# Performance work log

Hardware: AMD Instinct MI355X
Metric: run time of the kernel (lower is better)

The kernel has to match this reference:

```python
import jax, jax.numpy as jnp
import numpy as np

# Config (matches init_kwargs)
B, C, H, W = 32, 128, 12, 1200   # z: (B, in_dim, H, W)
DIN = C * H                       # 1536
FIX = 768                         # get_multiple(DIN // 2, 6)
OV = 4                            # overlap
G = 6                             # num_vqs
D = OV * FIX // G                 # 512 per-group embedding size (all equal)
K = 1024                          # codebook_size
COMMIT = 0.25


def setup_inputs() -> dict:
    key = jax.random.key(0)
    k1, k2, k3, k4 = jax.random.split(key, 4)
    z = jax.random.normal(k1, (B, C, H, W), dtype=jnp.float32)
    w_down = jax.random.normal(k2, (FIX, DIN), dtype=jnp.float32) * 0.02
    w_up = jax.random.normal(k3, (DIN, FIX), dtype=jnp.float32) * 0.02
    embedding = jax.random.normal(k4, (G, D, K), dtype=jnp.float32)  # per-group (embedding_size, num_embedding)
    return {"z": z, "w_down": w_down, "w_up": w_up, "embedding": embedding}


def _quantize_group(zg, emb):
    # zg: (B, T, D), emb: (D, K)
    zf = zg.reshape(-1, D)
    # squared euclidean distance: |z|^2 - 2 z@E + |E|^2 -> (N, K)
    dist = (zf * zf).sum(1, keepdims=True) - 2.0 * (zf @ emb) + (emb * emb).sum(0, keepdims=True)
    idx = jnp.argmin(dist, axis=1)            # (N,)
    q = jnp.take(emb.T, idx, axis=0).reshape(zg.shape)
    # straight-through estimator (training mode)
    zq = zg + jax.lax.stop_gradient(q - zg)
    loss = COMMIT * jnp.mean((jax.lax.stop_gradient(zq) - zg) ** 2)
    return zq, loss


def reference(z, w_down, w_up, embedding):
    # pre_process: (B,C,H,W) -> permute(0,2,3,1) -> permute(0,2,3,1) -> (B, W, C*H)
    x = jnp.transpose(z, (0, 3, 1, 2)).reshape(B, W, DIN)  # (B, W, C, H) flattened
    x = x @ w_down.T                                       # proj_down -> (B, W, FIX)
    T = W // OV
    x = x.reshape(B, T, OV * FIX)                          # (B, T, 3072)
    # split into G contiguous groups of size D along last axis -> (G, B, T, D)
    xg = jnp.transpose(x.reshape(B, T, G, D), (2, 0, 1, 3))
    zq_g, losses = jax.vmap(_quantize_group)(xg, embedding)
    vq_loss = losses.sum() / G
    # concat groups back -> (B, T, G*D)
    zq = jnp.transpose(zq_g, (1, 2, 0, 3)).reshape(B, T, G * D)
    # post_process: un-overlap, proj_up, back to (B, C, H, W)
    zq = zq.reshape(B, W, FIX)
    zq = zq @ w_up.T                                       # (B, W, DIN)
    zq = zq.reshape(B, W, C, H)
    zq = jnp.transpose(zq, (0, 3, 1, 2))                   # (B, H, W, C)
    zq = jnp.transpose(zq, (0, 3, 1, 2))                   # dim==4 -> (B, C, H, W)
    return zq, vq_loss
```

## Files before the change

### kernel.cpp

```cpp
#include <hip/hip_runtime.h>

#define BB 32
#define CC 128
#define HH 12
#define WW 1200
#define DIN 1536
#define FIXD 768
#define OVL 4
#define GG 6
#define DD 512
#define KK 1024
#define TT 300
#define NV 9600
#define MROWS 38400

#define Y_OFF     0
#define ET_OFF    29491200
#define NORM_OFF  32636928
#define BEST_OFF  32643072
#define LOSS_OFF  32758272

__global__ __launch_bounds__(256) void k_gemm_down(const float* __restrict__ z,
                                                   const float* __restrict__ w_down,
                                                   float* __restrict__ Y) {
    __shared__ float As[16][68];
    __shared__ float Bs[16][132];
    const int bm = blockIdx.x, bn = blockIdx.y;
    const int tid = threadIdx.x;
    const int n0 = bm * 64, f0 = bn * 128;
    const int arow = tid & 63;
    const int akk0 = tid >> 6;
    const int nA = n0 + arow;
    const int bA = nA / WW, wA = nA - bA * WW;
    const size_t zbase = (size_t)bA * (CC * HH * WW) + wA;
    const int rbase = (tid >> 4) << 2;
    const int cbase = (tid & 15) << 3;
    float acc[4][8] = {};
    for (int kt = 0; kt < DIN; kt += 16) {
        #pragma unroll
        for (int i = 0; i < 4; i++) {
            int kk = akk0 + i * 4;
            As[kk][arow] = z[zbase + (size_t)(kt + kk) * WW];
        }
        #pragma unroll
        for (int i = 0; i < 2; i++) {
            int fl = tid + i * 256;
            int col = fl >> 2, q = fl & 3;
            const float4 v = *(const float4*)&w_down[(size_t)(f0 + col) * DIN + kt + q * 4];
            Bs[q * 4 + 0][col] = v.x;
            Bs[q * 4 + 1][col] = v.y;
            Bs[q * 4 + 2][col] = v.z;
            Bs[q * 4 + 3][col] = v.w;
        }
        __syncthreads();
        #pragma unroll
        for (int k = 0; k < 16; k++) {
            const float4 a  = *(const float4*)&As[k][rbase];
            const float4 ba = *(const float4*)&Bs[k][cbase];
            const float4 bb = *(const float4*)&Bs[k][cbase + 4];
            const float av[4] = {a.x, a.y, a.z, a.w};
            const float bv[8] = {ba.x, ba.y, ba.z, ba.w, bb.x, bb.y, bb.z, bb.w};
            #pragma unroll
            for (int i = 0; i < 4; i++)
                #pragma unroll
                for (int j = 0; j < 8; j++)
                    acc[i][j] = fmaf(av[i], bv[j], acc[i][j]);
        }
        __syncthreads();
    }
    #pragma unroll
    for (int i = 0; i < 4; i++) {
        float4 o0, o1;
        o0.x = acc[i][0]; o0.y = acc[i][1]; o0.z = acc[i][2]; o0.w = acc[i][3];
        o1.x = acc[i][4]; o1.y = acc[i][5]; o1.z = acc[i][6]; o1.w = acc[i][7];
        float* yr = &Y[(size_t)(n0 + rbase + i) * FIXD + f0 + cbase];
        *(float4*)yr = o0;
        *(float4*)(yr + 4) = o1;
    }
}

__global__ __launch_bounds__(256) void k_transpose(const float* __restrict__ emb,
                                                   float* __restrict__ ET) {
    int i = blockIdx.x * 256 + threadIdx.x;
    if (i >= GG * KK * DD) return;
    int d = i & 511;
    int rem = i >> 9;
    int k = rem & 1023;
    int g = rem >> 10;
    ET[i] = emb[((g * DD + d) << 10) + k];
}

__global__ __launch_bounds__(64) void k_norms(const float* __restrict__ ET,
                                              float* __restrict__ norms) {
    const int code = blockIdx.x;
    const int lane = threadIdx.x;
    const float* row = ET + code * DD;
    double s = 0.0;
    #pragma unroll
    for (int r = 0; r < 8; r++) {
        float v = row[lane + r * 64];
        s += (double)v * (double)v;
    }
    #pragma unroll
    for (int off = 32; off; off >>= 1) s += __shfl_down(s, off);
    if (lane == 0) norms[code] = (float)s;
}

__global__ __launch_bounds__(256) void k_dist2(const float* __restrict__ Y,
                                               const float* __restrict__ ET,
                                               const float* __restrict__ norms,
                                               unsigned long long* __restrict__ best) {
    __shared__ float Zs[16][68];
    __shared__ float Es[16][132];
    __shared__ unsigned long long red[64][17];
    const int vt = blockIdx.x;
    const int ct = blockIdx.y;
    const int g  = blockIdx.z;
    const int tid = threadIdx.x;
    const int rgrp = tid >> 4, cgrp = tid & 15;
    const int rbase = rgrp * 4, cbase = cgrp * 8;
    const int v0 = vt * 64, c0 = ct * 128;
    const float* ETg = ET + (size_t)g * KK * DD;

    const int zrow = tid >> 2, zq = tid & 3;
    const int vz = v0 + zrow;
    const int bz = vz / TT, tz = vz - bz * TT;

    float acc[4][8] = {};

    for (int kt = 0; kt < DD; kt += 16) {
        const int p0 = g * DD + kt;
        const int s = p0 / FIXD, f0 = p0 - s * FIXD;
        {
            const float4 v = *(const float4*)&Y[(bz * WW + tz * OVL + s) * FIXD + f0 + zq * 4];
            Zs[zq * 4 + 0][zrow] = v.x;
            Zs[zq * 4 + 1][zrow] = v.y;
            Zs[zq * 4 + 2][zrow] = v.z;
            Zs[zq * 4 + 3][zrow] = v.w;
        }
        #pragma unroll
        for (int i = 0; i < 2; i++) {
            int flat = tid + i * 256;
            int code = flat >> 2, q = flat & 3;
            const float4 v = *(const float4*)&ETg[(c0 + code) * DD + kt + q * 4];
            Es[q * 4 + 0][code] = v.x;
            Es[q * 4 + 1][code] = v.y;
            Es[q * 4 + 2][code] = v.z;
            Es[q * 4 + 3][code] = v.w;
        }
        __syncthreads();
        #pragma unroll
        for (int k = 0; k < 16; k++) {
            const float4 z4 = *(const float4*)&Zs[k][rbase];
            const float4 ea = *(const float4*)&Es[k][cbase];
            const float4 eb = *(const float4*)&Es[k][cbase + 4];
            const float zv[4] = {z4.x, z4.y, z4.z, z4.w};
            const float ev[8] = {ea.x, ea.y, ea.z, ea.w, eb.x, eb.y, eb.z, eb.w};
            #pragma unroll
            for (int i = 0; i < 4; i++)
                #pragma unroll
                for (int j = 0; j < 8; j++)
                    acc[i][j] = fmaf(zv[i], ev[j], acc[i][j]);
        }
        __syncthreads();
    }

    unsigned long long kbest[4];
    #pragma unroll
    for (int i = 0; i < 4; i++) kbest[i] = ~0ull;
    #pragma unroll
    for (int j = 0; j < 8; j++) {
        const int c = c0 + cbase + j;
        const float nrm = norms[(g << 10) + c];
        #pragma unroll
        for (int i = 0; i < 4; i++) {
            float score = nrm - 2.0f * acc[i][j];
            unsigned u = __float_as_uint(score);
            u = (u & 0x80000000u) ? ~u : (u | 0x80000000u);
            unsigned long long key = ((unsigned long long)u << 32) | (unsigned)c;
            if (key < kbest[i]) kbest[i] = key;
        }
    }
    #pragma unroll
    for (int i = 0; i < 4; i++) red[rbase + i][cgrp] = kbest[i];
    __syncthreads();
    if (tid < 64) {
        unsigned long long b = red[tid][0];
        #pragma unroll
        for (int j = 1; j < 16; j++) {
            unsigned long long v = red[tid][j];
            if (v < b) b = v;
        }
        atomicMin(&best[g * NV + v0 + tid], b);
    }
}

__global__ __launch_bounds__(256) void k_loss(const float* __restrict__ Y,
                                              const float* __restrict__ ET,
                                              const unsigned long long* __restrict__ best,
                                              float* __restrict__ lossAcc) {
    const int total = GG * NV * DD;
    const int stride = gridDim.x * 256;
    float s = 0.0f;
    for (int e = blockIdx.x * 256 + threadIdx.x; e < total; e += stride) {
        int g = e / (NV * DD);
        int r = e - g * (NV * DD);
        int v = r >> 9, d = r & 511;
        int ii = (int)(unsigned)best[g * NV + v];
        float q = ET[((size_t)(g * KK + ii)) * DD + d];
        int b = v / TT, t = v - b * TT;
        int p = g * DD + d;
        int sg = p / FIXD, f = p - sg * FIXD;
        float zv = Y[(b * WW + t * OVL + sg) * FIXD + f];
        float df = q - zv;
        s = fmaf(df, df, s);
    }
    __shared__ float red[256];
    red[threadIdx.x] = s;
    __syncthreads();
    for (int off = 128; off; off >>= 1) {
        if (threadIdx.x < off) red[threadIdx.x] += red[threadIdx.x + off];
        __syncthreads();
    }
    if (threadIdx.x == 0) atomicAdd(lossAcc, red[0]);
}

__constant__ int SEG_G[8]  = {0, 1, 1, 2, 3, 4, 4, 5};
__constant__ int SEG_D0[8] = {0, 0, 256, 0, 0, 0, 256, 0};
__constant__ int SEG_L[8]  = {512, 256, 256, 512, 512, 256, 256, 512};
__constant__ int SEG_F0[8] = {0, 512, 0, 256, 0, 512, 0, 256};

__global__ __launch_bounds__(256) void k_table(const float* __restrict__ ET,
                                               const float* __restrict__ w_up,
                                               float* __restrict__ Tab) {
    __shared__ float As[16][68];
    __shared__ float Bs[16][132];
    const int bm = blockIdx.x;
    const int bn = blockIdx.y;
    const int seg = blockIdx.z;
    const int g = SEG_G[seg], d0 = SEG_D0[seg], len = SEG_L[seg], fb = SEG_F0[seg];
    const int tid = threadIdx.x;
    const int k0 = bm * 64, dout0 = bn * 128;
    const int arow = tid >> 2, aq = tid & 3;
    const int rbase = (tid >> 4) << 2;
    const int cbase = (tid & 15) << 3;
    const float* ETg = ET + (size_t)(g << 10) * DD;
    float acc[4][8] = {};
    for (int kt = 0; kt < len; kt += 16) {
        {
            const float4 v = *(const float4*)&ETg[(size_t)(k0 + arow) * DD + d0 + kt + aq * 4];
            As[aq * 4 + 0][arow] = v.x;
            As[aq * 4 + 1][arow] = v.y;
            As[aq * 4 + 2][arow] = v.z;
            As[aq * 4 + 3][arow] = v.w;
        }
        #pragma unroll
        for (int i = 0; i < 2; i++) {
            int fl = tid + i * 256;
            int col = fl >> 2, q = fl & 3;
            const float4 v = *(const float4*)&w_up[(size_t)(dout0 + col) * FIXD + fb + kt + q * 4];
            Bs[q * 4 + 0][col] = v.x;
            Bs[q * 4 + 1][col] = v.y;
            Bs[q * 4 + 2][col] = v.z;
            Bs[q * 4 + 3][col] = v.w;
        }
        __syncthreads();
        #pragma unroll
        for (int k = 0; k < 16; k++) {
            const float4 a  = *(const float4*)&As[k][rbase];
            const float4 ba = *(const float4*)&Bs[k][cbase];
            const float4 bb = *(const float4*)&Bs[k][cbase + 4];
            const float av[4] = {a.x, a.y, a.z, a.w};
            const float bv[8] = {ba.x, ba.y, ba.z, ba.w, bb.x, bb.y, bb.z, bb.w};
            #pragma unroll
            for (int i = 0; i < 4; i++)
                #pragma unroll
                for (int j = 0; j < 8; j++)
                    acc[i][j] = fmaf(av[i], bv[j], acc[i][j]);
        }
        __syncthreads();
    }
    #pragma unroll
    for (int i = 0; i < 4; i++) {
        float4 o0, o1;
        o0.x = acc[i][0]; o0.y = acc[i][1]; o0.z = acc[i][2]; o0.w = acc[i][3];
        o1.x = acc[i][4]; o1.y = acc[i][5]; o1.z = acc[i][6]; o1.w = acc[i][7];
        float* tr = &Tab[(size_t)((seg << 10) + k0 + rbase + i) * DIN + dout0 + cbase];
        *(float4*)tr = o0;
        *(float4*)(tr + 4) = o1;
    }
}

__global__ __launch_bounds__(256) void k_scatter(const float* __restrict__ Tab,
                                                 const unsigned long long* __restrict__ best,
                                                 float* __restrict__ out) {
    __shared__ float Ls[64][65];
    const int dt = blockIdx.x;
    const int wt = blockIdx.y;
    const int b  = blockIdx.z;
    const int dout0 = dt * 64, w0 = wt * 64;
    const int wlim = (WW - w0 < 64) ? (WW - w0) : 64;
    const int tid = threadIdx.x;
    const int wi = tid >> 2, q = tid & 3;

    int se = 0;
    size_t rowE = 0, rowO = 0;
    if (wi < wlim) {
        const int w = w0 + wi;
        const int s = w & 3;
        const int t = w >> 2;
        const int gEt[4] = {0, 1, 3, 4};
        const int gOt[4] = {1, 2, 4, 5};
        int ce = (int)(unsigned)best[gEt[s] * NV + b * TT + t];
        int co = (int)(unsigned)best[gOt[s] * NV + b * TT + t];
        se = s;
        rowE = (size_t)(((2 * s) << 10) + ce) * DIN;
        rowO = (size_t)(((2 * s + 1) << 10) + co) * DIN;
    }
    if (wi < wlim) {
        #pragma unroll
        for (int rep = 0; rep < 4; rep++) {
            const int doff = rep * 16 + q * 4;
            const float4 a = *(const float4*)&Tab[rowE + dout0 + doff];
            const float4 c = *(const float4*)&Tab[rowO + dout0 + doff];
            Ls[wi][doff + 0] = a.x + c.x;
            Ls[wi][doff + 1] = a.y + c.y;
            Ls[wi][doff + 2] = a.z + c.z;
            Ls[wi][doff + 3] = a.w + c.w;
        }
    }
    __syncthreads();
    const size_t obase = (size_t)b * (CC * HH * WW) + (size_t)dout0 * WW + w0;
    #pragma unroll
    for (int i = 0; i < 16; i++) {
        int flat = tid + i * 256;
        int dr = flat >> 6, wj = flat & 63;
        if (wj < wlim) out[obase + (size_t)dr * WW + wj] = Ls[wj][dr];
    }
}

__global__ void k_finish(const float* __restrict__ lossAcc, float* __restrict__ out) {
    if (threadIdx.x == 0)
        out[58982400] = lossAcc[0] * (0.25f / 29491200.0f);
}

extern "C" void kernel_launch(void* const* d_in, const int* in_sizes, int n_in,
                              void* d_out, int out_size, void* d_ws, size_t ws_size,
                              hipStream_t stream) {
    const float* z      = (const float*)d_in[0];
    const float* w_down = (const float*)d_in[1];
    const float* w_up   = (const float*)d_in[2];
    const float* emb    = (const float*)d_in[3];
    float* out = (float*)d_out;

    float* ws    = (float*)d_ws;
    float* Y     = ws + Y_OFF;
    float* Tab   = ws + Y_OFF;
    float* ET    = ws + ET_OFF;
    float* norms = ws + NORM_OFF;
    unsigned long long* best = (unsigned long long*)(ws + BEST_OFF);
    float* lossA = ws + LOSS_OFF;

    hipMemsetAsync(best, 0xFF, (size_t)GG * NV * sizeof(unsigned long long), stream);
    hipMemsetAsync(lossA, 0, sizeof(float), stream);

    dim3 gdown(600, 6);
    k_gemm_down<<<gdown, 256, 0, stream>>>(z, w_down, Y);

    k_transpose<<<(GG * KK * DD + 255) / 256, 256, 0, stream>>>(emb, ET);
    k_norms<<<GG * KK, 64, 0, stream>>>(ET, norms);

    dim3 gdist(150, 8, GG);
    k_dist2<<<gdist, 256, 0, stream>>>(Y, ET, norms, best);

    k_loss<<<2048, 256, 0, stream>>>(Y, ET, best, lossA);

    dim3 gtab(16, 12, 8);
    k_table<<<gtab, 256, 0, stream>>>(ET, w_up, Tab);

    dim3 gsc(24, 19, 32);
    k_scatter<<<gsc, 256, 0, stream>>>(Tab, best, out);

    k_finish<<<1, 64, 0, stream>>>(lossA, out);
}
```

Before: 2.230 ms.

## Enlarge down-projection GEMM tile to 128x128 and vectorize per-row loss kernel

The down-projection GEMM tile grows from 64x128 to 128x128, with each thread now computing an 8x8 output block instead of 4x8. This raises arithmetic intensity and halves the grid, at the cost of more registers per thread. The loss kernel moves from a flat grid-stride loop with per-element divides to one 8-thread group per quantized vector, using float4 loads and a single index lookup. The scatter kernel is lightly tidied with no change in behaviour.

```diff
diff --git a/kernel.cpp b/kernel.cpp
--- a/kernel.cpp
+++ b/kernel.cpp
@@ -23,45 +23,43 @@
 __global__ __launch_bounds__(256) void k_gemm_down(const float* __restrict__ z,
                                                    const float* __restrict__ w_down,
                                                    float* __restrict__ Y) {
-    __shared__ float As[16][68];
+    __shared__ float As[16][132];
     __shared__ float Bs[16][132];
-    const int bm = blockIdx.x, bn = blockIdx.y;
-    const int tid = threadIdx.x;
-    const int n0 = bm * 64, f0 = bn * 128;
-    const int arow = tid & 63;
-    const int akk0 = tid >> 6;
+    const int n0 = blockIdx.x * 128, f0 = blockIdx.y * 128;
+    const int tid = threadIdx.x;
+    const int arow = tid & 127;
+    const int ak0 = tid >> 7;
     const int nA = n0 + arow;
     const int bA = nA / WW, wA = nA - bA * WW;
     const size_t zbase = (size_t)bA * (CC * HH * WW) + wA;
-    const int rbase = (tid >> 4) << 2;
-    const int cbase = (tid & 15) << 3;
-    float acc[4][8] = {};
+    const int bcol = tid >> 1, bq = tid & 1;
+    const int trow = tid >> 4, tcol = tid & 15;
+    float acc[8][8] = {};
     for (int kt = 0; kt < DIN; kt += 16) {
         #pragma unroll
-        for (int i = 0; i < 4; i++) {
-            int kk = akk0 + i * 4;
+        for (int i = 0; i < 8; i++) {
+            const int kk = ak0 + i * 2;
             As[kk][arow] = z[zbase + (size_t)(kt + kk) * WW];
         }
         #pragma unroll
         for (int i = 0; i < 2; i++) {
-            int fl = tid + i * 256;
-            int col = fl >> 2, q = fl & 3;
-            const float4 v = *(const float4*)&w_down[(size_t)(f0 + col) * DIN + kt + q * 4];
-            Bs[q * 4 + 0][col] = v.x;
-            Bs[q * 4 + 1][col] = v.y;
-            Bs[q * 4 + 2][col] = v.z;
-            Bs[q * 4 + 3][col] = v.w;
+            const int q = bq + i * 2;
+            const float4 v = *(const float4*)&w_down[(size_t)(f0 + bcol) * DIN + kt + q * 4];
+            Bs[q * 4 + 0][bcol] = v.x;
+            Bs[q * 4 + 1][bcol] = v.y;
+            Bs[q * 4 + 2][bcol] = v.z;
+            Bs[q * 4 + 3][bcol] = v.w;
         }
         __syncthreads();
         #pragma unroll
         for (int k = 0; k < 16; k++) {
-            const float4 a  = *(const float4*)&As[k][rbase];
-            const float4 ba = *(const float4*)&Bs[k][cbase];
-            const float4 bb = *(const float4*)&Bs[k][cbase + 4];
-            const float av[4] = {a.x, a.y, a.z, a.w};
-            const float bv[8] = {ba.x, ba.y, ba.z, ba.w, bb.x, bb.y, bb.z, bb.w};
+            float av[8], bv[8];
+            *(float4*)&av[0] = *(const float4*)&As[k][trow * 8];
+            *(float4*)&av[4] = *(const float4*)&As[k][trow * 8 + 4];
+            *(float4*)&bv[0] = *(const float4*)&Bs[k][tcol * 8];
+            *(float4*)&bv[4] = *(const float4*)&Bs[k][tcol * 8 + 4];
             #pragma unroll
-            for (int i = 0; i < 4; i++)
+            for (int i = 0; i < 8; i++)
                 #pragma unroll
                 for (int j = 0; j < 8; j++)
                     acc[i][j] = fmaf(av[i], bv[j], acc[i][j]);
@@ -69,11 +67,11 @@
         __syncthreads();
     }
     #pragma unroll
-    for (int i = 0; i < 4; i++) {
+    for (int i = 0; i < 8; i++) {
         float4 o0, o1;
         o0.x = acc[i][0]; o0.y = acc[i][1]; o0.z = acc[i][2]; o0.w = acc[i][3];
         o1.x = acc[i][4]; o1.y = acc[i][5]; o1.z = acc[i][6]; o1.w = acc[i][7];
-        float* yr = &Y[(size_t)(n0 + rbase + i) * FIXD + f0 + cbase];
+        float* yr = &Y[(size_t)(n0 + trow * 8 + i) * FIXD + f0 + tcol * 8];
         *(float4*)yr = o0;
         *(float4*)(yr + 4) = o1;
     }
@@ -199,30 +197,34 @@
                                               const float* __restrict__ ET,
                                               const unsigned long long* __restrict__ best,
                                               float* __restrict__ lossAcc) {
-    const int total = GG * NV * DD;
-    const int stride = gridDim.x * 256;
+    const int tid = threadIdx.x;
+    const int v = blockIdx.x * 32 + (tid >> 3);
+    const int q = tid & 7;
+    const int g = v / NV;
+    const int r = v - g * NV;
+    const int b = r / TT, t = r - b * TT;
+    const int ii = (int)(unsigned)best[v];
+    const float* et = &ET[((size_t)((g << 10) + ii)) * DD];
     float s = 0.0f;
-    for (int e = blockIdx.x * 256 + threadIdx.x; e < total; e += stride) {
-        int g = e / (NV * DD);
-        int r = e - g * (NV * DD);
-        int v = r >> 9, d = r & 511;
-        int ii = (int)(unsigned)best[g * NV + v];
-        float q = ET[((size_t)(g * KK + ii)) * DD + d];
-        int b = v / TT, t = v - b * TT;
-        int p = g * DD + d;
-        int sg = p / FIXD, f = p - sg * FIXD;
-        float zv = Y[(b * WW + t * OVL + sg) * FIXD + f];
-        float df = q - zv;
-        s = fmaf(df, df, s);
+    #pragma unroll
+    for (int j = 0; j < 16; j++) {
+        const int d = j * 32 + q * 4;
+        const int p = g * DD + d;
+        const int sg = p / FIXD, f = p - sg * FIXD;
+        const float4 qv = *(const float4*)&et[d];
+        const float4 zv = *(const float4*)&Y[(size_t)(b * WW + t * OVL + sg) * FIXD + f];
+        float d0 = qv.x - zv.x, d1 = qv.y - zv.y, d2 = qv.z - zv.z, d3 = qv.w - zv.w;
+        s = fmaf(d0, d0, s); s = fmaf(d1, d1, s);
+        s = fmaf(d2, d2, s); s = fmaf(d3, d3, s);
     }
     __shared__ float red[256];
-    red[threadIdx.x] = s;
+    red[tid] = s;
     __syncthreads();
     for (int off = 128; off; off >>= 1) {
-        if (threadIdx.x < off) red[threadIdx.x] += red[threadIdx.x + off];
-        __syncthreads();
-    }
-    if (threadIdx.x == 0) atomicAdd(lossAcc, red[0]);
+        if (tid < off) red[tid] += red[tid + off];
+        __syncthreads();
+    }
+    if (tid == 0) atomicAdd(lossAcc, red[0]);
 }
 
 __constant__ int SEG_G[8]  = {0, 1, 1, 2, 3, 4, 4, 5};
@@ -303,8 +305,6 @@
     const int tid = threadIdx.x;
     const int wi = tid >> 2, q = tid & 3;
 
-    int se = 0;
-    size_t rowE = 0, rowO = 0;
     if (wi < wlim) {
         const int w = w0 + wi;
         const int s = w & 3;
@@ -313,11 +313,8 @@
         const int gOt[4] = {1, 2, 4, 5};
         int ce = (int)(unsigned)best[gEt[s] * NV + b * TT + t];
         int co = (int)(unsigned)best[gOt[s] * NV + b * TT + t];
-        se = s;
-        rowE = (size_t)(((2 * s) << 10) + ce) * DIN;
-        rowO = (size_t)(((2 * s + 1) << 10) + co) * DIN;
-    }
-    if (wi < wlim) {
+        size_t rowE = (size_t)(((2 * s) << 10) + ce) * DIN;
+        size_t rowO = (size_t)(((2 * s + 1) << 10) + co) * DIN;
         #pragma unroll
         for (int rep = 0; rep < 4; rep++) {
             const int doff = rep * 16 + q * 4;
@@ -364,7 +361,7 @@
     hipMemsetAsync(best, 0xFF, (size_t)GG * NV * sizeof(unsigned long long), stream);
     hipMemsetAsync(lossA, 0, sizeof(float), stream);
 
-    dim3 gdown(600, 6);
+    dim3 gdown(300, 6);
     k_gemm_down<<<gdown, 256, 0, stream>>>(z, w_down, Y);
 
     k_transpose<<<(GG * KK * DD + 255) / 256, 256, 0, stream>>>(emb, ET);
@@ -373,7 +370,7 @@
     dim3 gdist(150, 8, GG);
     k_dist2<<<gdist, 256, 0, stream>>>(Y, ET, norms, best);
 
-    k_loss<<<2048, 256, 0, stream>>>(Y, ET, best, lossA);
+    k_loss<<<1800, 256, 0, stream>>>(Y, ET, best, lossA);
 
     dim3 gtab(16, 12, 8);
     k_table<<<gtab, 256, 0, stream>>>(ET, w_up, Tab);
```

Measured after the change: 2.152 ms. 3.5% less time.
